# Kernel tuning notes

Measured on AMD Instinct MI355X. Metric: run time of the kernel, lower is better.

Reference implementation:

```python
import jax, jax.numpy as jnp
import numpy as np

B, N_IN, N_OUT, N, L, T_SS = 256, 1024, 256, 2048, 4, 32


def setup_inputs() -> dict:
    key = jax.random.key(0)
    ks = jax.random.split(key, 7)
    s_in = 1.0 / np.sqrt(N_IN)
    s_rec = 1.0 / np.sqrt(N)
    return {
        "X": jax.random.normal(ks[0], (B, N_IN), jnp.float32),
        "W_in_w": jax.random.uniform(ks[1], (N, N_IN), jnp.float32, -s_in, s_in),
        "W_in_b": jax.random.uniform(ks[2], (N,), jnp.float32, -s_in, s_in),
        "W_rec_w": jax.random.uniform(ks[3], (L, N, N), jnp.float32, -s_rec, s_rec),
        "W_rec_b": jax.random.uniform(ks[4], (L, N), jnp.float32, -s_rec, s_rec),
        "W_out_w": jax.random.uniform(ks[5], (N_OUT, N), jnp.float32, -s_rec, s_rec),
        "W_out_b": jax.random.uniform(ks[6], (N_OUT,), jnp.float32, -s_rec, s_rec),
        "T": T_SS,
    }


def reference(X, W_in_w, W_in_b, W_rec_w, W_rec_b, W_out_w, W_out_b, T):
    x_in = X @ W_in_w.T + W_in_b  # (B, N)
    h0 = jnp.zeros((L, X.shape[0], N), X.dtype)

    def step(h, _):
        # layer 0 driven by input projection; layers l>0 driven by layer l-1
        new0 = jnp.sin(x_in + h[0] @ W_rec_w[0].T + W_rec_b[0])
        hs = [new0]
        for l in range(1, L):
            hs.append(jnp.sin(hs[-1] + h[l] @ W_rec_w[l].T + W_rec_b[l]))
        return jnp.stack(hs), None

    h_final, _ = jax.lax.scan(step, h0, None, length=T)
    return h_final[-1] @ W_out_w.T + W_out_b
```

## Files before the change

### kernel.cpp

```cpp
#include <hip/hip_runtime.h>

typedef unsigned short u16;
typedef unsigned char u8;
typedef unsigned int u32;
typedef __bf16 bf16x8 __attribute__((ext_vector_type(8)));
typedef float f32x4 __attribute__((ext_vector_type(4)));
typedef u32 u32x4 __attribute__((ext_vector_type(4)));
typedef u32 u32x2 __attribute__((ext_vector_type(2)));
typedef u16 u16x4 __attribute__((ext_vector_type(4)));
typedef u16 u16x8 __attribute__((ext_vector_type(8)));
typedef int i32x4 __attribute__((ext_vector_type(4)));

#define NH 2048
#define BATCH 256
#define NIN 1024
#define NOUT 256
#define LAY 4
#define TSS 32
#define BK 64

#define SW_W 5747.0f
#define INV_DQ (1.0f / (127.0f * 5747.0f))

#define WAITVM(N) asm volatile("s_waitcnt vmcnt(" #N ")" ::: "memory")

__device__ __forceinline__ u16 f2bf(float f) {
  u32 u = __builtin_bit_cast(u32, f);
  u = (u + 0x7FFFu + ((u >> 16) & 1u)) >> 16;
  return (u16)u;
}
__device__ __forceinline__ float bf2f(u16 h) {
  u32 u = ((u32)h) << 16;
  return __builtin_bit_cast(float, u);
}

__device__ __forceinline__ float fast_sin(float x) {
  float k = __builtin_rintf(x * 0.3183098861837907f);
  float r = __builtin_fmaf(k, -3.14159274101257324f, x);
  r = __builtin_fmaf(k, 8.742277657347586e-08f, r);
  float s = r * r;
  float p = __builtin_fmaf(s, 2.75573192e-06f, -1.98412698e-04f);
  p = __builtin_fmaf(s, p, 8.33333333e-03f);
  p = __builtin_fmaf(s, p, -1.66666667e-01f);
  p = r + r * s * p;
  int ki = (int)k;
  return (ki & 1) ? -p : p;
}

__device__ __forceinline__ bf16x8 ld_frag(const u16* p) {
  u32x4 r = *(const u32x4*)p;
  return __builtin_bit_cast(bf16x8, r);
}

__device__ __forceinline__ f32x4 mfma16(bf16x8 a, bf16x8 b, f32x4 c) {
  return __builtin_amdgcn_mfma_f32_16x16x32_bf16(a, b, c, 0, 0, 0);
}

__device__ __forceinline__ i32x4 mfma_i8(i32x4 a, i32x4 b, i32x4 c) {
  return __builtin_amdgcn_mfma_i32_16x16x64_i8(a, b, c, 0, 0, 0);
}

__device__ __forceinline__ void gload16(const void* g, void* lds) {
  __builtin_amdgcn_global_load_lds(
      (__attribute__((address_space(1))) u32*)g,
      (__attribute__((address_space(3))) u32*)lds, 16, 0, 0);
}


__global__ __launch_bounds__(256) void k_cvt_w8(const float* __restrict__ in,
                                                u32* __restrict__ out, int n4) {
  int i = blockIdx.x * 256 + threadIdx.x;
  if (i >= n4) return;
  f32x4 v = ((const f32x4*)in)[i];
  u32 o = 0;
  #pragma unroll
  for (int j = 0; j < 4; j++) {
    int q = (int)__builtin_rintf(v[j] * SW_W);
    o |= ((u32)(q & 255)) << (8 * j);
  }
  out[i] = o;
}

__global__ __launch_bounds__(256) void k_split2(const float* __restrict__ in,
                                                u16* __restrict__ hi,
                                                u16* __restrict__ lo, int n4) {
  int i = blockIdx.x * 256 + threadIdx.x;
  if (i >= n4) return;
  f32x4 v = ((const f32x4*)in)[i];
  u16x4 hv, lv;
  #pragma unroll
  for (int j = 0; j < 4; j++) {
    u16 h = f2bf(v[j]);
    hv[j] = h;
    lv[j] = f2bf(v[j] - bf2f(h));
  }
  ((u16x4*)hi)[i] = hv;
  ((u16x4*)lo)[i] = lv;
}


struct GemmArgs {
  const u16* A[4];
  const u16* B[4];
  void* G;
  int ldA, ldB, kiters, nl;
};

template <int OBF, int NKS>
__global__ __launch_bounds__(256, 2) void k_gemm(GemmArgs args) {
  __shared__ alignas(16) u16 Ab[2][128 * BK];
  __shared__ alignas(16) u16 Bb[2][128 * BK];

  int bid = blockIdx.x;
  int nl = args.nl;
  int l = bid % nl;
  int t1 = bid / nl;
  int ks = t1 & (NKS - 1);
  int t2 = t1 / NKS;
  int nt = t2 & 15;
  int mt = t2 >> 4;

  int tid = threadIdx.x;
  int w = tid >> 6, lane = tid & 63;
  int l15 = lane & 15, l4 = lane >> 4;
  int ldA = args.ldA, ldB = args.ldB;
  int kiters = args.kiters;

  const u16* Ag = args.A[l] + (size_t)(mt * 128) * ldA + ks * (kiters * BK);
  const u16* Bg = args.B[l] + (size_t)(nt * 128) * ldB + ks * (kiters * BK);

  int srow = w * 32 + (lane >> 3);
  int csrc = ((lane & 7) ^ (lane >> 3)) * 8;
  int agoff[4], bgoff[4], lbase[4];
  #pragma unroll
  for (int j = 0; j < 4; j++) {
    agoff[j] = (srow + j * 8) * ldA + csrc;
    bgoff[j] = (srow + j * 8) * ldB + csrc;
    lbase[j] = w * 2048 + j * 512;
  }

  int wr = w >> 1, wc = w & 1;

  f32x4 zero = {0.f, 0.f, 0.f, 0.f};
  f32x4 acc[4][4];
  #pragma unroll
  for (int m = 0; m < 4; m++)
    #pragma unroll
    for (int n = 0; n < 4; n++) acc[m][n] = zero;

  auto stage = [&](int bufi, int kb) {
    int k0 = kb * BK;
    #pragma unroll
    for (int j = 0; j < 4; j++) {
      gload16(Ag + agoff[j] + k0, &Ab[bufi][lbase[j]]);
      gload16(Bg + bgoff[j] + k0, &Bb[bufi][lbase[j]]);
    }
  };
  auto compute = [&](int bufi) {
    #pragma unroll
    for (int kk = 0; kk < 2; kk++) {
      int swz = ((kk * 4 + l4) ^ (l15 & 7)) * 8;
      bf16x8 a[4], b[4];
      #pragma unroll
      for (int m = 0; m < 4; m++)
        a[m] = ld_frag(&Ab[bufi][(wr * 64 + m * 16 + l15) * BK + swz]);
      #pragma unroll
      for (int n = 0; n < 4; n++)
        b[n] = ld_frag(&Bb[bufi][(wc * 64 + n * 16 + l15) * BK + swz]);
      #pragma unroll
      for (int m = 0; m < 4; m++)
        #pragma unroll
        for (int n = 0; n < 4; n++)
          acc[m][n] = mfma16(a[m], b[n], acc[m][n]);
    }
  };

  stage(0, 0);
  stage(1, 1);

  int cur = 0;
  for (int kb = 0; kb < kiters - 2; kb++) {
    WAITVM(8);
    __builtin_amdgcn_s_barrier();
    compute(cur);
    __builtin_amdgcn_s_barrier();
    stage(cur, kb + 2);
    cur ^= 1;
  }
  WAITVM(8);
  __builtin_amdgcn_s_barrier();
  compute(cur);
  cur ^= 1;
  WAITVM(0);
  __builtin_amdgcn_s_barrier();
  compute(cur);

  size_t obase = ((size_t)(ks * nl + l) * BATCH + mt * 128) * NH + nt * 128;
  if (OBF) {
    u16* Go = (u16*)args.G + obase;
    #pragma unroll
    for (int m = 0; m < 4; m++) {
      int row = wr * 64 + m * 16 + l4 * 4;
      #pragma unroll
      for (int n = 0; n < 4; n++) {
        int col = wc * 64 + n * 16 + l15;
        #pragma unroll
        for (int r = 0; r < 4; r++)
          Go[(size_t)(row + r) * NH + col] = f2bf(acc[m][n][r]);
      }
    }
  } else {
    float* Go = (float*)args.G + obase;
    #pragma unroll
    for (int m = 0; m < 4; m++) {
      int row = wr * 64 + m * 16 + l4 * 4;
      #pragma unroll
      for (int n = 0; n < 4; n++) {
        int col = wc * 64 + n * 16 + l15;
        #pragma unroll
        for (int r = 0; r < 4; r++)
          Go[(size_t)(row + r) * NH + col] = acc[m][n][r];
      }
    }
  }
}


struct Rec8Args {
  const u8* h;
  const u8* W8;
  u16* Gp;
};

__global__ __launch_bounds__(256, 2) void k_gemm8(Rec8Args args) {
  __shared__ alignas(16) u8 Ab[2][128 * 128];
  __shared__ alignas(16) u8 Bb[2][128 * 128];

  int bid = blockIdx.x;
  int l = bid & 3;
  int ks = (bid >> 2) & 1;
  int nt = (bid >> 3) & 15;
  int mt = bid >> 7;

  int tid = threadIdx.x;
  int lane = tid & 63;
  int w = tid >> 6;
  int l15 = lane & 15, l4 = lane >> 4;
  int wr = w >> 1, wc = w & 1;

  const u8* Ag = args.h + (size_t)l * (BATCH * NH) + (size_t)(mt * 128) * NH + ks * 1024;
  const u8* Bg = args.W8 + (size_t)l * (NH * NH) + (size_t)(nt * 128) * NH + ks * 1024;

  int srow = tid >> 3;
  int csrc = ((tid & 7) ^ (srow & 7)) * 16;
  int goff[4], lbase[4];
  #pragma unroll
  for (int j = 0; j < 4; j++) {
    goff[j] = (j * 32 + srow) * NH + csrc;
    lbase[j] = j * 4096 + tid * 16;
  }

  i32x4 zero = {0, 0, 0, 0};
  i32x4 acc[4][4];
  #pragma unroll
  for (int m = 0; m < 4; m++)
    #pragma unroll
    for (int n = 0; n < 4; n++) acc[m][n] = zero;

  auto stage = [&](int bufi, int kb) {
    int k0 = kb * 128;
    #pragma unroll
    for (int j = 0; j < 4; j++) {
      gload16(Ag + goff[j] + k0, &Ab[bufi][lbase[j]]);
      gload16(Bg + goff[j] + k0, &Bb[bufi][lbase[j]]);
    }
  };
  auto compute = [&](int bufi) {
    #pragma unroll
    for (int kk = 0; kk < 2; kk++) {
      int swz = ((kk * 4 + l4) ^ (l15 & 7)) * 16;
      i32x4 a[4], b[4];
      #pragma unroll
      for (int m = 0; m < 4; m++)
        a[m] = *(const i32x4*)&Ab[bufi][(wr * 64 + m * 16 + l15) * 128 + swz];
      #pragma unroll
      for (int n = 0; n < 4; n++)
        b[n] = *(const i32x4*)&Bb[bufi][(wc * 64 + n * 16 + l15) * 128 + swz];
      #pragma unroll
      for (int m = 0; m < 4; m++)
        #pragma unroll
        for (int n = 0; n < 4; n++)
          acc[m][n] = mfma_i8(a[m], b[n], acc[m][n]);
    }
  };

  stage(0, 0);
  stage(1, 1);

  int cur = 0;
  #pragma unroll 1
  for (int kb = 0; kb < 6; kb++) {
    WAITVM(8);
    __builtin_amdgcn_s_barrier();
    compute(cur);
    __builtin_amdgcn_s_barrier();
    stage(cur, kb + 2);
    cur ^= 1;
  }
  WAITVM(8);
  __builtin_amdgcn_s_barrier();
  compute(cur);
  cur ^= 1;
  WAITVM(0);
  __builtin_amdgcn_s_barrier();
  compute(cur);

  u16* Go = args.Gp + (size_t)(ks * LAY + l) * (BATCH * NH) +
            (size_t)(mt * 128) * NH + nt * 128;
  #pragma unroll
  for (int m = 0; m < 4; m++) {
    int row = wr * 64 + m * 16 + l4 * 4;
    #pragma unroll
    for (int n = 0; n < 4; n++) {
      int col = wc * 64 + n * 16 + l15;
      #pragma unroll
      for (int r = 0; r < 4; r++)
        Go[(size_t)(row + r) * NH + col] = f2bf((float)acc[m][n][r] * INV_DQ);
    }
  }
}

__global__ __launch_bounds__(256) void k_chain8(const u16* __restrict__ Gp,
                                                const float* __restrict__ x_in,
                                                const float* __restrict__ brec,
                                                u8* __restrict__ hq,
                                                u16* __restrict__ h3bf) {
  int i = blockIdx.x * 256 + threadIdx.x;
  int e = i * 8;
  int col = e & (NH - 1);
  f32x4 p0 = *(const f32x4*)(x_in + e);
  f32x4 p1 = *(const f32x4*)(x_in + e + 4);
  #pragma unroll
  for (int l = 0; l < LAY; l++) {
    u16x8 g0 = *(const u16x8*)(Gp + (size_t)(0 * LAY + l) * (BATCH * NH) + e);
    u16x8 g1 = *(const u16x8*)(Gp + (size_t)(1 * LAY + l) * (BATCH * NH) + e);
    f32x4 b0 = *(const f32x4*)(brec + l * NH + col);
    f32x4 b1 = *(const f32x4*)(brec + l * NH + col + 4);
    u32x2 qw = {0u, 0u};
    u16x8 hv;
    #pragma unroll
    for (int j = 0; j < 4; j++) {
      float v = fast_sin(p0[j] + bf2f(g0[j]) + bf2f(g1[j]) + b0[j]);
      p0[j] = v;
      int q = (int)__builtin_rintf(v * 127.0f);
      qw[0] |= ((u32)(q & 255)) << (8 * j);
      hv[j] = f2bf(v);
    }
    #pragma unroll
    for (int j = 0; j < 4; j++) {
      float v = fast_sin(p1[j] + bf2f(g0[4 + j]) + bf2f(g1[4 + j]) + b1[j]);
      p1[j] = v;
      int q = (int)__builtin_rintf(v * 127.0f);
      qw[1] |= ((u32)(q & 255)) << (8 * j);
      hv[4 + j] = f2bf(v);
    }
    *(u32x2*)(hq + (size_t)l * (BATCH * NH) + e) = qw;
    if (l == LAY - 1) *(u16x8*)(h3bf + e) = hv;
  }
}

__global__ __launch_bounds__(256) void k_xin_fin(const float* __restrict__ Gp2,
                                                 const float* __restrict__ bin,
                                                 float* __restrict__ x_in) {
  int i = blockIdx.x * 256 + threadIdx.x;
  int e = i * 4;
  int col = e & (NH - 1);
  f32x4 s = *(const f32x4*)(bin + col);
  #pragma unroll
  for (int t = 0; t < 6; t++)
    s += *(const f32x4*)(Gp2 + (size_t)t * (BATCH * NH) + e);
  *(f32x4*)(x_in + e) = s;
}

__global__ __launch_bounds__(64) void k_gemm_out(const u16* __restrict__ h3,
                                                 const u16* __restrict__ Wh,
                                                 const u16* __restrict__ Wl,
                                                 const float* __restrict__ bout,
                                                 float* __restrict__ out) {
  int bid = blockIdx.x;
  int mt = bid & 7, nt = bid >> 3;
  int lane = threadIdx.x;
  int l15 = lane & 15, l4 = lane >> 4;
  f32x4 zero = {0.f, 0.f, 0.f, 0.f};
  f32x4 acc0 = zero, acc1 = zero;
  const u16* a0p = h3 + (size_t)(mt * 32 + l15) * NH + l4 * 8;
  const u16* a1p = a0p + 16 * NH;
  const u16* bhp = Wh + (size_t)(nt * 16 + l15) * NH + l4 * 8;
  const u16* blp = Wl + (size_t)(nt * 16 + l15) * NH + l4 * 8;
  for (int kb = 0; kb < 64; kb++) {
    bf16x8 a0 = ld_frag(a0p + kb * 32);
    bf16x8 a1 = ld_frag(a1p + kb * 32);
    bf16x8 bh = ld_frag(bhp + kb * 32);
    bf16x8 bl = ld_frag(blp + kb * 32);
    acc0 = mfma16(a0, bh, acc0);
    acc0 = mfma16(a0, bl, acc0);
    acc1 = mfma16(a1, bh, acc1);
    acc1 = mfma16(a1, bl, acc1);
  }
  float bo = bout[nt * 16 + l15];
  #pragma unroll
  for (int r = 0; r < 4; r++) {
    out[(size_t)(mt * 32 + l4 * 4 + r) * NOUT + nt * 16 + l15] = acc0[r] + bo;
    out[(size_t)(mt * 32 + 16 + l4 * 4 + r) * NOUT + nt * 16 + l15] = acc1[r] + bo;
  }
}


extern "C" void kernel_launch(void* const* d_in, const int* in_sizes, int n_in,
                              void* d_out, int out_size, void* d_ws, size_t ws_size,
                              hipStream_t stream) {
  const float* X     = (const float*)d_in[0];
  const float* Winw  = (const float*)d_in[1];
  const float* Winb  = (const float*)d_in[2];
  const float* Wrw   = (const float*)d_in[3];
  const float* Wrb   = (const float*)d_in[4];
  const float* Woutw = (const float*)d_in[5];
  const float* Woutb = (const float*)d_in[6];
  float* out = (float*)d_out;

  char* ws = (char*)d_ws;
  u8*  W8     = (u8*)(ws);
  u8*  h0i    = (u8*)(ws + 16777216);
  u8*  h1i    = (u8*)(ws + 18874368);
  u16* h3bf   = (u16*)(ws + 20971520);
  float* xin  = (float*)(ws + 22020096);
  u16* Gp     = (u16*)(ws + 24117248);
  float* Gp2  = (float*)(ws + 32505856);
  u16* Xhi    = (u16*)(ws + 45088768);
  u16* Xlo    = (u16*)(ws + 45613056);
  u16* Winh   = (u16*)(ws + 46137344);
  u16* Winl   = (u16*)(ws + 50331648);
  u16* Wouth  = (u16*)(ws + 54525952);
  u16* Woutl  = (u16*)(ws + 55574528);

  k_cvt_w8<<<16384, 256, 0, stream>>>(Wrw, (u32*)W8, 4194304);
  k_split2<<<256, 256, 0, stream>>>(X, Xhi, Xlo, 65536);
  k_split2<<<2048, 256, 0, stream>>>(Winw, Winh, Winl, 524288);
  k_split2<<<512, 256, 0, stream>>>(Woutw, Wouth, Woutl, 131072);
  hipMemsetAsync(h0i, 0, 2097152, stream);

  GemmArgs ax;
  ax.A[0] = Xhi; ax.A[1] = Xhi; ax.A[2] = Xlo; ax.A[3] = Xhi;
  ax.B[0] = Winh; ax.B[1] = Winl; ax.B[2] = Winh; ax.B[3] = Winh;
  ax.G = Gp2; ax.ldA = NIN; ax.ldB = NIN; ax.kiters = 8; ax.nl = 3;
  k_gemm<0, 2><<<192, 256, 0, stream>>>(ax);
  k_xin_fin<<<512, 256, 0, stream>>>(Gp2, Winb, xin);

  u8* hin = h0i;
  u8* hout = h1i;
  for (int t = 0; t < TSS; t++) {
    Rec8Args ar;
    ar.h = hin; ar.W8 = W8; ar.Gp = Gp;
    k_gemm8<<<256, 256, 0, stream>>>(ar);
    k_chain8<<<256, 256, 0, stream>>>(Gp, xin, Wrb, hout, h3bf);
    u8* tmp = hin; hin = hout; hout = tmp;
  }

  k_gemm_out<<<128, 64, 0, stream>>>(h3bf, Wouth, Woutl, Woutb, out);
}
```

Baseline: 596.0 us.

## Replace split-K recurrent GEMM with 64x128 tiles over full K

```diff
diff --git a/kernel.cpp b/kernel.cpp
--- a/kernel.cpp
+++ b/kernel.cpp
@@ -233,14 +233,13 @@
 };
 
 __global__ __launch_bounds__(256, 2) void k_gemm8(Rec8Args args) {
-  __shared__ alignas(16) u8 Ab[2][128 * 128];
+  __shared__ alignas(16) u8 Ab[2][64 * 128];
   __shared__ alignas(16) u8 Bb[2][128 * 128];
 
   int bid = blockIdx.x;
   int l = bid & 3;
-  int ks = (bid >> 2) & 1;
-  int nt = (bid >> 3) & 15;
-  int mt = bid >> 7;
+  int mt = (bid >> 2) & 3;
+  int nt = bid >> 4;
 
   int tid = threadIdx.x;
   int lane = tid & 63;
@@ -248,46 +247,52 @@
   int l15 = lane & 15, l4 = lane >> 4;
   int wr = w >> 1, wc = w & 1;
 
-  const u8* Ag = args.h + (size_t)l * (BATCH * NH) + (size_t)(mt * 128) * NH + ks * 1024;
-  const u8* Bg = args.W8 + (size_t)l * (NH * NH) + (size_t)(nt * 128) * NH + ks * 1024;
+  const u8* Ag = args.h + (size_t)l * (BATCH * NH) + (size_t)(mt * 64) * NH;
+  const u8* Bg = args.W8 + (size_t)l * (NH * NH) + (size_t)(nt * 128) * NH;
 
   int srow = tid >> 3;
   int csrc = ((tid & 7) ^ (srow & 7)) * 16;
-  int goff[4], lbase[4];
+  int goffA[2], lbaseA[2], goffB[4], lbaseB[4];
+  #pragma unroll
+  for (int j = 0; j < 2; j++) {
+    goffA[j] = (j * 32 + srow) * NH + csrc;
+    lbaseA[j] = j * 4096 + tid * 16;
+  }
   #pragma unroll
   for (int j = 0; j < 4; j++) {
-    goff[j] = (j * 32 + srow) * NH + csrc;
-    lbase[j] = j * 4096 + tid * 16;
+    goffB[j] = (j * 32 + srow) * NH + csrc;
+    lbaseB[j] = j * 4096 + tid * 16;
   }
 
   i32x4 zero = {0, 0, 0, 0};
-  i32x4 acc[4][4];
-  #pragma unroll
-  for (int m = 0; m < 4; m++)
+  i32x4 acc[2][4];
+  #pragma unroll
+  for (int m = 0; m < 2; m++)
     #pragma unroll
     for (int n = 0; n < 4; n++) acc[m][n] = zero;
 
   auto stage = [&](int bufi, int kb) {
     int k0 = kb * 128;
     #pragma unroll
-    for (int j = 0; j < 4; j++) {
-      gload16(Ag + goff[j] + k0, &Ab[bufi][lbase[j]]);
-      gload16(Bg + goff[j] + k0, &Bb[bufi][lbase[j]]);
-    }
+    for (int j = 0; j < 2; j++)
+      gload16(Ag + goffA[j] + k0, &Ab[bufi][lbaseA[j]]);
+    #pragma unroll
+    for (int j = 0; j < 4; j++)
+      gload16(Bg + goffB[j] + k0, &Bb[bufi][lbaseB[j]]);
   };
   auto compute = [&](int bufi) {
     #pragma unroll
     for (int kk = 0; kk < 2; kk++) {
       int swz = ((kk * 4 + l4) ^ (l15 & 7)) * 16;
-      i32x4 a[4], b[4];
-      #pragma unroll
-      for (int m = 0; m < 4; m++)
-        a[m] = *(const i32x4*)&Ab[bufi][(wr * 64 + m * 16 + l15) * 128 + swz];
+      i32x4 a[2], b[4];
+      #pragma unroll
+      for (int m = 0; m < 2; m++)
+        a[m] = *(const i32x4*)&Ab[bufi][(wr * 32 + m * 16 + l15) * 128 + swz];
       #pragma unroll
       for (int n = 0; n < 4; n++)
         b[n] = *(const i32x4*)&Bb[bufi][(wc * 64 + n * 16 + l15) * 128 + swz];
       #pragma unroll
-      for (int m = 0; m < 4; m++)
+      for (int m = 0; m < 2; m++)
         #pragma unroll
         for (int n = 0; n < 4; n++)
           acc[m][n] = mfma_i8(a[m], b[n], acc[m][n]);
@@ -299,15 +304,15 @@
 
   int cur = 0;
   #pragma unroll 1
-  for (int kb = 0; kb < 6; kb++) {
-    WAITVM(8);
+  for (int kb = 0; kb < 14; kb++) {
+    WAITVM(6);
     __builtin_amdgcn_s_barrier();
     compute(cur);
     __builtin_amdgcn_s_barrier();
     stage(cur, kb + 2);
     cur ^= 1;
   }
-  WAITVM(8);
+  WAITVM(6);
   __builtin_amdgcn_s_barrier();
   compute(cur);
   cur ^= 1;
@@ -315,11 +320,11 @@
   __builtin_amdgcn_s_barrier();
   compute(cur);
 
-  u16* Go = args.Gp + (size_t)(ks * LAY + l) * (BATCH * NH) +
-            (size_t)(mt * 128) * NH + nt * 128;
-  #pragma unroll
-  for (int m = 0; m < 4; m++) {
-    int row = wr * 64 + m * 16 + l4 * 4;
+  u16* Go = args.Gp + (size_t)l * (BATCH * NH) + (size_t)(mt * 64) * NH +
+            nt * 128;
+  #pragma unroll
+  for (int m = 0; m < 2; m++) {
+    int row = wr * 32 + m * 16 + l4 * 4;
     #pragma unroll
     for (int n = 0; n < 4; n++) {
       int col = wc * 64 + n * 16 + l15;
@@ -342,15 +347,14 @@
   f32x4 p1 = *(const f32x4*)(x_in + e + 4);
   #pragma unroll
   for (int l = 0; l < LAY; l++) {
-    u16x8 g0 = *(const u16x8*)(Gp + (size_t)(0 * LAY + l) * (BATCH * NH) + e);
-    u16x8 g1 = *(const u16x8*)(Gp + (size_t)(1 * LAY + l) * (BATCH * NH) + e);
+    u16x8 g0 = *(const u16x8*)(Gp + (size_t)l * (BATCH * NH) + e);
     f32x4 b0 = *(const f32x4*)(brec + l * NH + col);
     f32x4 b1 = *(const f32x4*)(brec + l * NH + col + 4);
     u32x2 qw = {0u, 0u};
     u16x8 hv;
     #pragma unroll
     for (int j = 0; j < 4; j++) {
-      float v = fast_sin(p0[j] + bf2f(g0[j]) + bf2f(g1[j]) + b0[j]);
+      float v = fast_sin(p0[j] + bf2f(g0[j]) + b0[j]);
       p0[j] = v;
       int q = (int)__builtin_rintf(v * 127.0f);
       qw[0] |= ((u32)(q & 255)) << (8 * j);
@@ -358,7 +362,7 @@
     }
     #pragma unroll
     for (int j = 0; j < 4; j++) {
-      float v = fast_sin(p1[j] + bf2f(g0[4 + j]) + bf2f(g1[4 + j]) + b1[j]);
+      float v = fast_sin(p1[j] + bf2f(g0[4 + j]) + b1[j]);
       p1[j] = v;
       int q = (int)__builtin_rintf(v * 127.0f);
       qw[1] |= ((u32)(q & 255)) << (8 * j);
@@ -435,13 +439,13 @@
   u16* h3bf   = (u16*)(ws + 20971520);
   float* xin  = (float*)(ws + 22020096);
   u16* Gp     = (u16*)(ws + 24117248);
-  float* Gp2  = (float*)(ws + 32505856);
-  u16* Xhi    = (u16*)(ws + 45088768);
-  u16* Xlo    = (u16*)(ws + 45613056);
-  u16* Winh   = (u16*)(ws + 46137344);
-  u16* Winl   = (u16*)(ws + 50331648);
-  u16* Wouth  = (u16*)(ws + 54525952);
-  u16* Woutl  = (u16*)(ws + 55574528);
+  float* Gp2  = (float*)(ws + 28311552);
+  u16* Xhi    = (u16*)(ws + 40894464);
+  u16* Xlo    = (u16*)(ws + 41418752);
+  u16* Winh   = (u16*)(ws + 41943040);
+  u16* Winl   = (u16*)(ws + 46137344);
+  u16* Wouth  = (u16*)(ws + 50331648);
+  u16* Woutl  = (u16*)(ws + 51380224);
 
   k_cvt_w8<<<16384, 256, 0, stream>>>(Wrw, (u32*)W8, 4194304);
   k_split2<<<256, 256, 0, stream>>>(X, Xhi, Xlo, 65536);
```

New measurement: 591.6 us. No clear change (-0.8%).
